# Kernel tuning notes

Measured on AMD Instinct MI355X. Metric: run time of the kernel, lower is better.

## Reference

```python
import jax, jax.numpy as jnp
import numpy as np

N = 10000          # in_size: number of nodes
H = 8              # n_heads
D = 64             # dimension per head
FEAT = H * D       # 512, node feature width (heads concatenated)
N_NETS = 3         # number of input networks (modalities)
E = 160000         # edges per network


def setup_inputs() -> dict:
    key = jax.random.key(0)
    ks = jax.random.split(key, 6)
    x = jax.random.normal(ks[0], (N, FEAT), dtype=jnp.float32)
    # n_id: global node ids in the sampled data_flow (here: full graph, identity)
    n_id = jnp.arange(N, dtype=jnp.int32)
    # per-network GAT attention values (non-negative, like softmaxed attn)
    attns = jax.random.uniform(ks[1], (N_NETS, E, H), dtype=jnp.float32)
    # per-network global edge indices (row 0 = source, row 1 = target)
    edges_global = jax.random.randint(ks[2], (N_NETS, 2, E), 0, N, dtype=jnp.int32)
    # learned per-head, per-network combination weights: net_weights[:, net_idx]
    net_weights = jax.random.uniform(ks[3], (H, N_NETS), dtype=jnp.float32)
    # ComboWGATConv linear: in = dimension*n_heads, out = dimension per head (concat)
    W = jax.random.normal(ks[4], (FEAT, FEAT), dtype=jnp.float32) * 0.02
    bias = jnp.zeros((FEAT,), dtype=jnp.float32)
    return {"x": x, "n_id": n_id, "attns": attns, "edges_global": edges_global,
            "net_weights": net_weights, "W": W, "bias": bias}


def reference(x, n_id, attns, edges_global, net_weights, W, bias):
    n_nodes, feat = x.shape
    n_nets, e, h = attns.shape
    d = feat // h

    # --- multi-network attention combination (aggregat_edge_weights) ---
    # w_cogat_attn[i] = net_weights[:, i] * attns[i]   -> (nets, E, H)
    w_attn = attns * net_weights.T[:, None, :]
    # Sparse add/coalesce across modalities: since the subsequent scatter-sum is
    # linear in edge weights, summing duplicate edges is equivalent to keeping
    # the concatenated (non-coalesced) edge list. nets-major flatten order.
    agg_alpha = w_attn.reshape(n_nets * e, h)                      # (Etot, H)
    agg_edges = edges_global.transpose(1, 0, 2).reshape(2, n_nets * e)  # (2, Etot)

    # --- edge_idx_from_global_to_local: invert n_id lookup ---
    inv = jnp.zeros((N,), dtype=jnp.int32).at[n_id].set(
        jnp.arange(n_nodes, dtype=jnp.int32))
    src = inv[agg_edges[0]]
    dst = inv[agg_edges[1]]

    # --- ComboWGATConv with externally supplied alpha (layer_no == 0) ---
    x_l = x[n_id]                                   # gather subgraph features
    hfeat = (x_l @ W).reshape(n_nodes, h, d)        # per-head transform
    msg = agg_alpha[:, :, None] * hfeat[src]        # (Etot, H, D) gather+weight
    out = jax.ops.segment_sum(msg, dst, num_segments=n_nodes)  # scatter-sum
    out = out.reshape(n_nodes, feat) + bias         # concat heads + bias
    return out
```

## Files before the change

kernel.cpp:

```cpp
#include <hip/hip_runtime.h>

#define NNODES 10000
#define NHEADS 8
#define DHEAD 64
#define FEAT 512
#define NNETS 3
#define EDGES 160000
#define ETOT (NNETS * EDGES)
#define NBUCK 4
#define BUCKSZ 2500
#define NKEY (NNODES * NBUCK)

#define CVTX_BLKS 5000
#define CVTW_BLKS 256
#define HIST_BLKS 1875
#define INV_BLKS 40

typedef unsigned short ushort_t;
typedef __bf16 bf16x8 __attribute__((ext_vector_type(8)));
typedef float f32x4 __attribute__((ext_vector_type(4)));
typedef unsigned u32x4 __attribute__((ext_vector_type(4)));

static __device__ __forceinline__ ushort_t f2b(float f) {
    unsigned u = __float_as_uint(f);
    unsigned r = u + 0x7FFF + ((u >> 16) & 1);
    return (ushort_t)(r >> 16);
}

static __device__ __forceinline__ void mfma16(f32x4& d, bf16x8 a, bf16x8 b) {
    asm volatile("v_mfma_f32_16x16x32_bf16 %0, %1, %2, %0" : "+v"(d) : "v"(a), "v"(b));
}

#define GLDS(gp, lp)                                                                     \
    __builtin_amdgcn_global_load_lds((const __attribute__((address_space(1))) void*)(gp), \
                                     (__attribute__((address_space(3))) void*)(lp), 16, 0, 0)

__global__ __launch_bounds__(256) void prep_fused_kernel(
    const float* __restrict__ x, ushort_t* __restrict__ xb, const float* __restrict__ W,
    ushort_t* __restrict__ wbt, const int* __restrict__ edges, int* __restrict__ counts,
    const int* __restrict__ n_id, int* __restrict__ inv) {
    __shared__ float tile[32][33];
    int b = blockIdx.x;
    int t = threadIdx.x;
    if (b < CVTX_BLKS) {
        int i = (b * 256 + t) * 4;
        float4 v = *(const float4*)(x + i);
        ushort4 o;
        o.x = f2b(v.x);
        o.y = f2b(v.y);
        o.z = f2b(v.z);
        o.w = f2b(v.w);
        *(ushort4*)(xb + i) = o;
    } else if (b < CVTX_BLKS + CVTW_BLKS) {
        int bb = b - CVTX_BLKS;
        int n0 = (bb & 15) * 32, k0 = (bb >> 4) * 32;
        int r = t >> 3, c4 = (t & 7) * 4;
        float4 v = *(const float4*)(&W[(size_t)(k0 + r) * FEAT + n0 + c4]);
        tile[r][c4 + 0] = v.x;
        tile[r][c4 + 1] = v.y;
        tile[r][c4 + 2] = v.z;
        tile[r][c4 + 3] = v.w;
        __syncthreads();
        ushort4 o;
        o.x = f2b(tile[c4 + 0][r]);
        o.y = f2b(tile[c4 + 1][r]);
        o.z = f2b(tile[c4 + 2][r]);
        o.w = f2b(tile[c4 + 3][r]);
        *(ushort4*)(&wbt[(size_t)(n0 + r) * FEAT + k0 + c4]) = o;
    } else if (b < CVTX_BLKS + CVTW_BLKS + HIST_BLKS) {
        int eid = (b - CVTX_BLKS - CVTW_BLKS) * 256 + t;
        int net = eid / EDGES;
        int e = eid - net * EDGES;
        int srcg = edges[net * (2 * EDGES) + e];
        int dstg = edges[net * (2 * EDGES) + EDGES + e];
        atomicAdd(&counts[dstg * NBUCK + srcg / BUCKSZ], 1);
    } else {
        int i = (b - CVTX_BLKS - CVTW_BLKS - HIST_BLKS) * 256 + t;
        if (i < NNODES) inv[n_id[i]] = i;
    }
}

__global__ __launch_bounds__(1024) void scan_kernel(const int* __restrict__ counts,
                                                    int* __restrict__ offsets) {
    __shared__ int wincl[16];
    int t = threadIdx.x;
    int ln = t & 63;
    int w = t >> 6;
    int4 v[10];
    int mysum = 0;
    if (t < 1000) {
        const int4* cp = (const int4*)(counts + t * 40);
#pragma unroll
        for (int i = 0; i < 10; ++i) {
            v[i] = cp[i];
            mysum += v[i].x + v[i].y + v[i].z + v[i].w;
        }
    }
    int s = mysum;
#pragma unroll
    for (int o = 1; o < 64; o <<= 1) {
        int u = __shfl_up(s, o, 64);
        if (ln >= o) s += u;
    }
    if (ln == 63) wincl[w] = s;
    __syncthreads();
    if (w == 0) {
        int ws = (ln < 16) ? wincl[ln] : 0;
#pragma unroll
        for (int o = 1; o < 16; o <<= 1) {
            int u = __shfl_up(ws, o, 64);
            if (ln >= o) ws += u;
        }
        if (ln < 16) wincl[ln] = ws;
    }
    __syncthreads();
    int base = ((w > 0) ? wincl[w - 1] : 0) + s - mysum;
    if (t < 1000) {
        int running = base;
        int* op = offsets + t * 40;
#pragma unroll
        for (int i = 0; i < 10; ++i) {
            op[i * 4 + 0] = running; running += v[i].x;
            op[i * 4 + 1] = running; running += v[i].y;
            op[i * 4 + 2] = running; running += v[i].z;
            op[i * 4 + 3] = running; running += v[i].w;
        }
        if (t == 999) offsets[NKEY] = running;
    }
}

__global__ __launch_bounds__(256) void scatter_kernel(const int* __restrict__ edges,
                                                      const int* __restrict__ inv,
                                                      const int* __restrict__ offsets,
                                                      int* __restrict__ cursor,
                                                      const float* __restrict__ attns,
                                                      const float* __restrict__ nw,
                                                      int* __restrict__ srcoff,
                                                      ushort_t* __restrict__ alphab) {
    int eid = blockIdx.x * 256 + threadIdx.x;
    int net = eid / EDGES;
    int e = eid - net * EDGES;
    int srcg = edges[net * (2 * EDGES) + e];
    int dstg = edges[net * (2 * EDGES) + EDGES + e];
    int key = dstg * NBUCK + srcg / BUCKSZ;
    int pos = offsets[key] + atomicAdd(&cursor[key], 1);
    srcoff[pos] = inv[srcg] << 10;
    float4 A0 = *(const float4*)(&attns[(size_t)eid * NHEADS]);
    float4 A1 = *(const float4*)(&attns[(size_t)eid * NHEADS + 4]);
    ushort4 o0, o1;
    o0.x = f2b(A0.x * nw[0 * NNETS + net]);
    o0.y = f2b(A0.y * nw[1 * NNETS + net]);
    o0.z = f2b(A0.z * nw[2 * NNETS + net]);
    o0.w = f2b(A0.w * nw[3 * NNETS + net]);
    o1.x = f2b(A1.x * nw[4 * NNETS + net]);
    o1.y = f2b(A1.y * nw[5 * NNETS + net]);
    o1.z = f2b(A1.z * nw[6 * NNETS + net]);
    o1.w = f2b(A1.w * nw[7 * NNETS + net]);
    *(ushort4*)(&alphab[(size_t)pos * NHEADS]) = o0;
    *(ushort4*)(&alphab[(size_t)pos * NHEADS + 4]) = o1;
}

__global__ __launch_bounds__(256) void gemm_mfma_kernel(const ushort_t* __restrict__ xb,
                                                        const ushort_t* __restrict__ wbt,
                                                        ushort_t* __restrict__ Cq) {
    __shared__ ushort_t Alds[128 * 32];
    __shared__ ushort_t Blds[128 * 32];
    const int t = threadIdx.x;
    const int wv = t >> 6;
    const int l = t & 63;
    const int lane15 = l & 15;
    const int hi = l >> 4;
    const int r0 = blockIdx.y * 128;
    const int c0 = blockIdx.x * 128;
    const int WR = (wv >> 1) * 64;
    const int WC = (wv & 1) * 64;

    const int srow = (wv << 4) + (l >> 2);
    const int scol = (l & 3) << 3;
    const ushort_t* Ab0 = xb + (size_t)min(r0 + srow, NNODES - 1) * FEAT + scol;
    const ushort_t* Ab1 = xb + (size_t)min(r0 + 64 + srow, NNODES - 1) * FEAT + scol;
    const ushort_t* Bb0 = wbt + (size_t)(c0 + srow) * FEAT + scol;
    const ushort_t* Bb1 = wbt + (size_t)(c0 + 64 + srow) * FEAT + scol;
    ushort_t* Al0 = &Alds[wv * 512];
    ushort_t* Al1 = &Alds[2048 + wv * 512];
    ushort_t* Bl0 = &Blds[wv * 512];
    ushort_t* Bl1 = &Blds[2048 + wv * 512];

    f32x4 acc[4][4] = {};

    for (int k0 = 0; k0 < FEAT; k0 += 32) {
        GLDS(Ab0 + k0, Al0);
        GLDS(Ab1 + k0, Al1);
        GLDS(Bb0 + k0, Bl0);
        GLDS(Bb1 + k0, Bl1);
        __syncthreads();
        bf16x8 a[4], b[4];
        const ushort_t* Ap = &Alds[(WR + lane15) * 32 + hi * 8];
        const ushort_t* Bp = &Blds[(WC + lane15) * 32 + hi * 8];
#pragma unroll
        for (int m = 0; m < 4; ++m) a[m] = *(const bf16x8*)(Ap + m * 512);
#pragma unroll
        for (int n = 0; n < 4; ++n) b[n] = *(const bf16x8*)(Bp + n * 512);
#pragma unroll
        for (int m = 0; m < 4; ++m)
#pragma unroll
            for (int n = 0; n < 4; ++n) mfma16(acc[m][n], a[m], b[n]);
        __syncthreads();
    }
    asm volatile("s_nop 7\n\ts_nop 7\n\ts_nop 7" ::);
    const int h = (c0 + WC) >> 6;
#pragma unroll
    for (int m = 0; m < 4; ++m) {
#pragma unroll
        for (int rr = 0; rr < 4; ++rr) {
            int row = r0 + WR + m * 16 + hi * 4 + rr;
            if (row < NNODES) {
#pragma unroll
                for (int n = 0; n < 4; ++n) {
                    int d = n * 16 + lane15;
                    Cq[(size_t)row * FEAT + d * NHEADS + h] = f2b(acc[m][n][rr]);
                }
            }
        }
    }
}

static __device__ __forceinline__ void fma_pair(unsigned a, unsigned h, float& lo,
                                                float& hi) {
    float alo = __uint_as_float(a << 16);
    float ahi = __uint_as_float(a & 0xFFFF0000u);
    float hlo = __uint_as_float(h << 16);
    float hhi = __uint_as_float(h & 0xFFFF0000u);
    lo = fmaf(alo, hlo, lo);
    hi = fmaf(ahi, hhi, hi);
}

__global__ __launch_bounds__(256) void aggregate_kernel(
    const int* __restrict__ srcoff, const int* __restrict__ offsets,
    const int* __restrict__ n_id, const u32x4* __restrict__ alf,
    const ushort_t* __restrict__ hfeatq, const float* __restrict__ bias,
    float* __restrict__ out) {
    int wv = threadIdx.x >> 6;
    int d = threadIdx.x & 63;
    const char* hb = (const char*)hfeatq + d * 16;
    int n = blockIdx.x * 4 + wv;
    int g = n_id[n];
    int beg = offsets[g * NBUCK], end = offsets[g * NBUCK + NBUCK];
    float acc[8] = {};
    int k = beg;
    for (; k + 8 <= end; k += 8) {
        u32x4 sA = *(const u32x4*)&srcoff[k];
        u32x4 sB = *(const u32x4*)&srcoff[k + 4];
        u32x4 gg[8], aa[8];
        gg[0] = *(const u32x4*)(hb + sA.x);
        gg[1] = *(const u32x4*)(hb + sA.y);
        gg[2] = *(const u32x4*)(hb + sA.z);
        gg[3] = *(const u32x4*)(hb + sA.w);
        gg[4] = *(const u32x4*)(hb + sB.x);
        gg[5] = *(const u32x4*)(hb + sB.y);
        gg[6] = *(const u32x4*)(hb + sB.z);
        gg[7] = *(const u32x4*)(hb + sB.w);
#pragma unroll
        for (int i = 0; i < 8; ++i) aa[i] = alf[k + i];
#pragma unroll
        for (int i = 0; i < 8; ++i) {
            fma_pair(aa[i].x, gg[i].x, acc[0], acc[1]);
            fma_pair(aa[i].y, gg[i].y, acc[2], acc[3]);
            fma_pair(aa[i].z, gg[i].z, acc[4], acc[5]);
            fma_pair(aa[i].w, gg[i].w, acc[6], acc[7]);
        }
    }
    for (; k < end; ++k) {
        unsigned so = *(const unsigned*)&srcoff[k];
        u32x4 a0 = alf[k];
        u32x4 g0 = *(const u32x4*)(hb + so);
        fma_pair(a0.x, g0.x, acc[0], acc[1]);
        fma_pair(a0.y, g0.y, acc[2], acc[3]);
        fma_pair(a0.z, g0.z, acc[4], acc[5]);
        fma_pair(a0.w, g0.w, acc[6], acc[7]);
    }
#pragma unroll
    for (int h = 0; h < NHEADS; ++h) {
        int c = h * DHEAD + d;
        __builtin_nontemporal_store(acc[h] + bias[c], &out[(size_t)n * FEAT + c]);
    }
}

extern "C" void kernel_launch(void* const* d_in, const int* in_sizes, int n_in,
                              void* d_out, int out_size, void* d_ws, size_t ws_size,
                              hipStream_t stream) {
    const float* x = (const float*)d_in[0];
    const int* n_id = (const int*)d_in[1];
    const float* attns = (const float*)d_in[2];
    const int* edges = (const int*)d_in[3];
    const float* nw = (const float*)d_in[4];
    const float* W = (const float*)d_in[5];
    const float* bias = (const float*)d_in[6];
    float* out = (float*)d_out;

    char* ws = (char*)d_ws;
    size_t o = 0;
    ushort_t* hfeatq = (ushort_t*)(ws + o); o += 10240000;
    ushort_t* alphab = (ushort_t*)(ws + o); o += 7680000;
    ushort_t* xb     = (ushort_t*)(ws + o); o += 10240000;
    ushort_t* wbt    = (ushort_t*)(ws + o); o += 524288;
    int* srcoff      = (int*)(ws + o);      o += 1920000;
    int* counts      = (int*)(ws + o);      o += 160000;
    int* cursor      = (int*)(ws + o);      o += 160000;
    int* offsets     = (int*)(ws + o);      o += 160004;
    int* inv         = (int*)(ws + o);      o += 40000;

    hipMemsetAsync(counts, 0, 320000, stream);
    prep_fused_kernel<<<CVTX_BLKS + CVTW_BLKS + HIST_BLKS + INV_BLKS, 256, 0, stream>>>(
        x, xb, W, wbt, edges, counts, n_id, inv);
    scan_kernel<<<1, 1024, 0, stream>>>(counts, offsets);
    scatter_kernel<<<HIST_BLKS, 256, 0, stream>>>(edges, inv, offsets, cursor, attns, nw,
                                                  srcoff, alphab);
    dim3 ggrid(FEAT / 128, (NNODES + 127) / 128);
    gemm_mfma_kernel<<<ggrid, 256, 0, stream>>>(xb, wbt, hfeatq);
    aggregate_kernel<<<NNODES / 4, 256, 0, stream>>>(srcoff, offsets, n_id,
                                                     (const u32x4*)alphab, hfeatq,
                                                     bias, out);
}
```

Measured before the change: 146.1 us.

## Merge edge scatter and GEMM into one launch with block-range dispatch

```diff
diff --git a/kernel.cpp b/kernel.cpp
--- a/kernel.cpp
+++ b/kernel.cpp
@@ -15,6 +15,8 @@
 #define CVTW_BLKS 256
 #define HIST_BLKS 1875
 #define INV_BLKS 40
+#define SCAT_BLKS 1875
+#define GEMM_BLKS 316
 
 typedef unsigned short ushort_t;
 typedef __bf16 bf16x8 __attribute__((ext_vector_type(8)));
@@ -129,49 +131,47 @@
     }
 }
 
-__global__ __launch_bounds__(256) void scatter_kernel(const int* __restrict__ edges,
-                                                      const int* __restrict__ inv,
-                                                      const int* __restrict__ offsets,
-                                                      int* __restrict__ cursor,
-                                                      const float* __restrict__ attns,
-                                                      const float* __restrict__ nw,
-                                                      int* __restrict__ srcoff,
-                                                      ushort_t* __restrict__ alphab) {
-    int eid = blockIdx.x * 256 + threadIdx.x;
-    int net = eid / EDGES;
-    int e = eid - net * EDGES;
-    int srcg = edges[net * (2 * EDGES) + e];
-    int dstg = edges[net * (2 * EDGES) + EDGES + e];
-    int key = dstg * NBUCK + srcg / BUCKSZ;
-    int pos = offsets[key] + atomicAdd(&cursor[key], 1);
-    srcoff[pos] = inv[srcg] << 10;
-    float4 A0 = *(const float4*)(&attns[(size_t)eid * NHEADS]);
-    float4 A1 = *(const float4*)(&attns[(size_t)eid * NHEADS + 4]);
-    ushort4 o0, o1;
-    o0.x = f2b(A0.x * nw[0 * NNETS + net]);
-    o0.y = f2b(A0.y * nw[1 * NNETS + net]);
-    o0.z = f2b(A0.z * nw[2 * NNETS + net]);
-    o0.w = f2b(A0.w * nw[3 * NNETS + net]);
-    o1.x = f2b(A1.x * nw[4 * NNETS + net]);
-    o1.y = f2b(A1.y * nw[5 * NNETS + net]);
-    o1.z = f2b(A1.z * nw[6 * NNETS + net]);
-    o1.w = f2b(A1.w * nw[7 * NNETS + net]);
-    *(ushort4*)(&alphab[(size_t)pos * NHEADS]) = o0;
-    *(ushort4*)(&alphab[(size_t)pos * NHEADS + 4]) = o1;
-}
-
-__global__ __launch_bounds__(256) void gemm_mfma_kernel(const ushort_t* __restrict__ xb,
-                                                        const ushort_t* __restrict__ wbt,
-                                                        ushort_t* __restrict__ Cq) {
+__global__ __launch_bounds__(256) void gemm_scatter_kernel(
+    const ushort_t* __restrict__ xb, const ushort_t* __restrict__ wbt,
+    ushort_t* __restrict__ Cq, const int* __restrict__ edges,
+    const int* __restrict__ inv, const int* __restrict__ offsets,
+    int* __restrict__ cursor, const float* __restrict__ attns,
+    const float* __restrict__ nw, int* __restrict__ srcoff,
+    ushort_t* __restrict__ alphab) {
+    const int t = threadIdx.x;
+    if (blockIdx.x < SCAT_BLKS) {
+        int eid = blockIdx.x * 256 + t;
+        int net = eid / EDGES;
+        int e = eid - net * EDGES;
+        int srcg = edges[net * (2 * EDGES) + e];
+        int dstg = edges[net * (2 * EDGES) + EDGES + e];
+        int key = dstg * NBUCK + srcg / BUCKSZ;
+        int pos = offsets[key] + atomicAdd(&cursor[key], 1);
+        srcoff[pos] = inv[srcg] << 10;
+        float4 A0 = *(const float4*)(&attns[(size_t)eid * NHEADS]);
+        float4 A1 = *(const float4*)(&attns[(size_t)eid * NHEADS + 4]);
+        ushort4 o0, o1;
+        o0.x = f2b(A0.x * nw[0 * NNETS + net]);
+        o0.y = f2b(A0.y * nw[1 * NNETS + net]);
+        o0.z = f2b(A0.z * nw[2 * NNETS + net]);
+        o0.w = f2b(A0.w * nw[3 * NNETS + net]);
+        o1.x = f2b(A1.x * nw[4 * NNETS + net]);
+        o1.y = f2b(A1.y * nw[5 * NNETS + net]);
+        o1.z = f2b(A1.z * nw[6 * NNETS + net]);
+        o1.w = f2b(A1.w * nw[7 * NNETS + net]);
+        *(ushort4*)(&alphab[(size_t)pos * NHEADS]) = o0;
+        *(ushort4*)(&alphab[(size_t)pos * NHEADS + 4]) = o1;
+        return;
+    }
     __shared__ ushort_t Alds[128 * 32];
     __shared__ ushort_t Blds[128 * 32];
-    const int t = threadIdx.x;
+    const int gb = blockIdx.x - SCAT_BLKS;
     const int wv = t >> 6;
     const int l = t & 63;
     const int lane15 = l & 15;
     const int hi = l >> 4;
-    const int r0 = blockIdx.y * 128;
-    const int c0 = blockIdx.x * 128;
+    const int r0 = (gb >> 2) * 128;
+    const int c0 = (gb & 3) * 128;
     const int WR = (wv >> 1) * 64;
     const int WC = (wv & 1) * 64;
 
@@ -314,10 +314,8 @@
     prep_fused_kernel<<<CVTX_BLKS + CVTW_BLKS + HIST_BLKS + INV_BLKS, 256, 0, stream>>>(
         x, xb, W, wbt, edges, counts, n_id, inv);
     scan_kernel<<<1, 1024, 0, stream>>>(counts, offsets);
-    scatter_kernel<<<HIST_BLKS, 256, 0, stream>>>(edges, inv, offsets, cursor, attns, nw,
-                                                  srcoff, alphab);
-    dim3 ggrid(FEAT / 128, (NNODES + 127) / 128);
-    gemm_mfma_kernel<<<ggrid, 256, 0, stream>>>(xb, wbt, hfeatq);
+    gemm_scatter_kernel<<<SCAT_BLKS + GEMM_BLKS, 256, 0, stream>>>(
+        xb, wbt, hfeatq, edges, inv, offsets, cursor, attns, nw, srcoff, alphab);
     aggregate_kernel<<<NNODES / 4, 256, 0, stream>>>(srcoff, offsets, n_id,
                                                      (const u32x4*)alphab, hfeatq,
                                                      bias, out);
```

Result: faster. 141.6 us (-3.1%).
